# Kernel optimization log

Measured on AMD Instinct MI355X. Metric: run time of the kernel, lower is better.

The kernel has to match this reference:

```python
import jax, jax.numpy as jnp
import numpy as np
import math

D_MODEL = 1024
N_HEADS = 16
D_HEAD = D_MODEL // N_HEADS
D_FF = 4 * D_MODEL
EPS = 1e-5


def layer_norm(x, gamma, beta):
    mu = jnp.mean(x, axis=-1, keepdims=True)
    var = jnp.var(x, axis=-1, keepdims=True)
    return (x - mu) * jax.lax.rsqrt(var + EPS) * gamma + beta


def setup_inputs() -> dict:
    key = jax.random.key(0)
    ks = jax.random.split(key, 8)
    B, C, D = 32, 256, D_MODEL
    s = 0.02
    return {
        "X": jax.random.normal(ks[0], (B, C, D), dtype=jnp.float32),
        "W_qkv": jax.random.normal(ks[1], (D, 3 * D), dtype=jnp.float32) * s,
        "b_qkv": jnp.zeros((3 * D,), dtype=jnp.float32),
        "W_proj": jax.random.normal(ks[2], (D, D), dtype=jnp.float32) * s,
        "b_proj": jnp.zeros((D,), dtype=jnp.float32),
        "g1": jnp.ones((D,), dtype=jnp.float32),
        "beta1": jnp.zeros((D,), dtype=jnp.float32),
        "g2": jnp.ones((D,), dtype=jnp.float32),
        "beta2": jnp.zeros((D,), dtype=jnp.float32),
        "W_ff1": jax.random.normal(ks[3], (D, D_FF), dtype=jnp.float32) * s,
        "b_ff1": jnp.zeros((D_FF,), dtype=jnp.float32),
        "W_ff2": jax.random.normal(ks[4], (D_FF, D), dtype=jnp.float32) * s,
        "b_ff2": jnp.zeros((D,), dtype=jnp.float32),
    }


def reference(X, W_qkv, b_qkv, W_proj, b_proj, g1, beta1, g2, beta2,
              W_ff1, b_ff1, W_ff2, b_ff2):
    B, C, D = X.shape
    H, Dh = N_HEADS, D_HEAD
    scale = 1.0 / math.sqrt(Dh)

    Xn = layer_norm(X, g1, beta1)
    qkv = Xn @ W_qkv + b_qkv                       # [B, C, 3D]
    q, k, v = jnp.split(qkv, 3, axis=-1)
    # split heads -> [B, H, C, Dh]
    sh = lambda t: t.reshape(B, C, H, Dh).transpose(0, 2, 1, 3)
    q, k, v = sh(q), sh(k), sh(v)

    scores = jnp.einsum("bhcd,bhkd->bhck", q, k) * scale  # [B, H, C, C]
    attn = jax.nn.softmax(scores, axis=-1)
    ctx = jnp.einsum("bhck,bhkd->bhcd", attn, v)           # [B, H, C, Dh]
    ctx = ctx.transpose(0, 2, 1, 3).reshape(B, C, D)

    X1 = X + (ctx @ W_proj + b_proj)
    X2n = layer_norm(X1, g2, beta2)
    h = jax.nn.gelu(X2n @ W_ff1 + b_ff1, approximate=False)
    X_out = X1 + (h @ W_ff2 + b_ff2)
    A = attn.mean(axis=1)                                   # [B, C, C]
    return (X_out, A)
```

## Files before the change

### kernel.cpp

```cpp
#include <hip/hip_runtime.h>
#include <cstdint>
#include <cstddef>

typedef short bf16x8 __attribute__((ext_vector_type(8)));
typedef float f32x4 __attribute__((ext_vector_type(4)));
typedef unsigned short u16;
typedef u16 u16x8 __attribute__((ext_vector_type(8)));

#define GLD16(gptr, lptr)                                                            \
  __builtin_amdgcn_global_load_lds((const __attribute__((address_space(1))) void*)(gptr), \
                                   (__attribute__((address_space(3))) void*)(lptr), 16, 0, 0)

__device__ __forceinline__ u16 f2bf(float f) {
  union { float f; unsigned u; } v; v.f = f;
  unsigned r = v.u + 0x7FFF + ((v.u >> 16) & 1);
  return (u16)(r >> 16);
}
__device__ __forceinline__ float bf2f(u16 h) {
  union { unsigned u; float f; } v; v.u = ((unsigned)h) << 16;
  return v.f;
}

template <int N> __device__ __forceinline__ void vmwait() {
  if constexpr (N == 0) asm volatile("s_waitcnt vmcnt(0)" ::: "memory");
  else if constexpr (N == 2) asm volatile("s_waitcnt vmcnt(2)" ::: "memory");
  else asm volatile("s_waitcnt vmcnt(8)" ::: "memory");
}

__device__ __forceinline__ f32x4 mfma16(bf16x8 a, bf16x8 b, f32x4 c) {
  return __builtin_amdgcn_mfma_f32_16x16x32_bf16(a, b, c, 0, 0, 0);
}

__device__ __forceinline__ bf16x8 lds_read_sw64(const u16* base, int row, int col) {
  int byt = row * 128 + col * 2;
  byt ^= (row & 7) << 4;
  return *(const bf16x8*)((const char*)base + byt);
}

__global__ __launch_bounds__(256) void transpose_cast(const float* __restrict__ in,
                                                      u16* __restrict__ out, int R, int C) {
  __shared__ float tile[32][33];
  const int tx = threadIdx.x, ty = threadIdx.y;
  const int c0 = blockIdx.x * 32, r0 = blockIdx.y * 32;
#pragma unroll
  for (int i = 0; i < 32; i += 8)
    tile[ty + i][tx] = in[(size_t)(r0 + ty + i) * C + c0 + tx];
  __syncthreads();
#pragma unroll
  for (int i = 0; i < 32; i += 8)
    out[(size_t)(c0 + ty + i) * R + r0 + tx] = f2bf(tile[tx][ty + i]);
}

__global__ __launch_bounds__(256) void layernorm_bf16(const float* __restrict__ X,
                                                      const float* __restrict__ g,
                                                      const float* __restrict__ be,
                                                      u16* __restrict__ out) {
  const int row = blockIdx.x, t = threadIdx.x;
  const int lane = t & 63, wave = t >> 6;
  const float* x = X + (size_t)row * 1024;
  __shared__ float part[4];
  float v[4]; float s = 0.f;
#pragma unroll
  for (int i = 0; i < 4; ++i) { v[i] = x[t + i * 256]; s += v[i]; }
#pragma unroll
  for (int o = 32; o >= 1; o >>= 1) s += __shfl_xor(s, o);
  if (lane == 0) part[wave] = s;
  __syncthreads();
  const float mu = (part[0] + part[1] + part[2] + part[3]) * (1.f / 1024.f);
  float d2 = 0.f;
#pragma unroll
  for (int i = 0; i < 4; ++i) { float d = v[i] - mu; d2 += d * d; }
#pragma unroll
  for (int o = 32; o >= 1; o >>= 1) d2 += __shfl_xor(d2, o);
  __syncthreads();
  if (lane == 0) part[wave] = d2;
  __syncthreads();
  const float var = (part[0] + part[1] + part[2] + part[3]) * (1.f / 1024.f);
  const float rstd = rsqrtf(var + 1e-5f);
#pragma unroll
  for (int i = 0; i < 4; ++i) {
    const int c = t + i * 256;
    out[(size_t)row * 1024 + c] = f2bf((v[i] - mu) * rstd * g[c] + be[c]);
  }
}

template <int EPI>
__global__ __launch_bounds__(512, 2) void gemm_4p(const u16* __restrict__ A,
                                                  const u16* __restrict__ Bt,
                                                  const float* __restrict__ bias,
                                                  const float* __restrict__ res,
                                                  float* __restrict__ outf,
                                                  u16* __restrict__ outb,
                                                  int M, int N, int K) {
  constexpr int TSZ = 256 * 128;
  __shared__ __attribute__((aligned(16))) char lds[4 * TSZ];

  const int t = threadIdx.x, lane = t & 63, wave = t >> 6;
  const int wm = wave >> 2, wn = wave & 3;
  const int l15 = lane & 15, l16 = lane >> 4;

  const int lb = ((int)blockIdx.x & 7) * ((int)gridDim.x >> 3) + ((int)blockIdx.x >> 3);
  const int NBN = N >> 8;
  const int bm = (lb / NBN) * 256, bn = (lb % NBN) * 256;

  const u16* aptr[4];
  const u16* bptr[4];
#pragma unroll
  for (int u = 0; u < 4; ++u) {
    int Lb = u * 8192 + t * 16;
    int x = (Lb ^ ((Lb >> 3) & 0x70)) >> 1;
    aptr[u] = A + (size_t)(bm + (x >> 6)) * K + (x & 63);
    bptr[u] = Bt + (size_t)(bn + (x >> 6)) * K + (x & 63);
  }
  auto stA = [&](int p, int u) { GLD16(aptr[u] + p * 64, lds + (p & 1) * TSZ + u * 8192 + t * 16); };
  auto stB = [&](int p, int u) { GLD16(bptr[u] + p * 64, lds + 2 * TSZ + (p & 1) * TSZ + u * 8192 + t * 16); };

  stA(0, 0); stA(0, 2); stB(0, 0); stB(0, 1); stB(0, 2); stB(0, 3); stA(0, 1); stA(0, 3);

  f32x4 acc[8][4] = {};
  const int nkt = K >> 6;

#pragma unroll 1
  for (int kt = 0; kt < nkt; ++kt) {
    const char* ab = lds + (kt & 1) * TSZ;
    const char* bb = lds + 2 * TSZ + (kt & 1) * TSZ;
    const bool st = (kt + 1 < nkt);
    bf16x8 aF[4][2], b0[2][2], b1[2][2];

    vmwait<2>();
    asm volatile("s_barrier" ::: "memory");
    if (st) { stA(kt + 1, 0); stA(kt + 1, 2); stB(kt + 1, 0); stB(kt + 1, 1); }
#pragma unroll
    for (int fm = 0; fm < 4; ++fm) {
      const int r = wm * 128 + fm * 16 + l15;
      const int rb = r * 128, sw = (r & 7) << 4;
      aF[fm][0] = *(const bf16x8*)(ab + rb + ((l16 * 16) ^ sw));
      aF[fm][1] = *(const bf16x8*)(ab + rb + ((64 + l16 * 16) ^ sw));
    }
#pragma unroll
    for (int fn = 0; fn < 2; ++fn) {
      const int r = wn * 64 + fn * 16 + l15;
      const int rb = r * 128, sw = (r & 7) << 4;
      b0[fn][0] = *(const bf16x8*)(bb + rb + ((l16 * 16) ^ sw));
      b0[fn][1] = *(const bf16x8*)(bb + rb + ((64 + l16 * 16) ^ sw));
    }
    asm volatile("s_waitcnt lgkmcnt(0)" ::: "memory");
    __builtin_amdgcn_sched_barrier(0);
    __builtin_amdgcn_s_setprio(1);
#pragma unroll
    for (int ks = 0; ks < 2; ++ks)
#pragma unroll
      for (int fm = 0; fm < 4; ++fm)
#pragma unroll
        for (int fn = 0; fn < 2; ++fn)
          acc[fm][fn] = mfma16(aF[fm][ks], b0[fn][ks], acc[fm][fn]);
    __builtin_amdgcn_s_setprio(0);

    asm volatile("s_barrier" ::: "memory");
    if (st) { stB(kt + 1, 2); stB(kt + 1, 3); stA(kt + 1, 1); stA(kt + 1, 3); }
#pragma unroll
    for (int fn = 0; fn < 2; ++fn) {
      const int r = wn * 64 + (2 + fn) * 16 + l15;
      const int rb = r * 128, sw = (r & 7) << 4;
      b1[fn][0] = *(const bf16x8*)(bb + rb + ((l16 * 16) ^ sw));
      b1[fn][1] = *(const bf16x8*)(bb + rb + ((64 + l16 * 16) ^ sw));
    }
    asm volatile("s_waitcnt lgkmcnt(0)" ::: "memory");
    __builtin_amdgcn_sched_barrier(0);
    __builtin_amdgcn_s_setprio(1);
#pragma unroll
    for (int ks = 0; ks < 2; ++ks)
#pragma unroll
      for (int fm = 0; fm < 4; ++fm)
#pragma unroll
        for (int fn = 0; fn < 2; ++fn)
          acc[fm][2 + fn] = mfma16(aF[fm][ks], b1[fn][ks], acc[fm][2 + fn]);
    __builtin_amdgcn_s_setprio(0);

    if (st) vmwait<8>(); else vmwait<0>();
    asm volatile("s_barrier" ::: "memory");
#pragma unroll
    for (int fm = 0; fm < 4; ++fm) {
      const int r = wm * 128 + (4 + fm) * 16 + l15;
      const int rb = r * 128, sw = (r & 7) << 4;
      aF[fm][0] = *(const bf16x8*)(ab + rb + ((l16 * 16) ^ sw));
      aF[fm][1] = *(const bf16x8*)(ab + rb + ((64 + l16 * 16) ^ sw));
    }
    asm volatile("s_waitcnt lgkmcnt(0)" ::: "memory");
    __builtin_amdgcn_sched_barrier(0);
    __builtin_amdgcn_s_setprio(1);
#pragma unroll
    for (int ks = 0; ks < 2; ++ks)
#pragma unroll
      for (int fm = 0; fm < 4; ++fm)
#pragma unroll
        for (int fn = 0; fn < 2; ++fn)
          acc[4 + fm][2 + fn] = mfma16(aF[fm][ks], b1[fn][ks], acc[4 + fm][2 + fn]);
    __builtin_amdgcn_s_setprio(0);

    __builtin_amdgcn_s_setprio(1);
#pragma unroll
    for (int ks = 0; ks < 2; ++ks)
#pragma unroll
      for (int fm = 0; fm < 4; ++fm)
#pragma unroll
        for (int fn = 0; fn < 2; ++fn)
          acc[4 + fm][fn] = mfma16(aF[fm][ks], b0[fn][ks], acc[4 + fm][fn]);
    __builtin_amdgcn_s_setprio(0);
  }

  const int r0 = l16 * 4;
#pragma unroll
  for (int fm = 0; fm < 8; ++fm) {
#pragma unroll
    for (int fn = 0; fn < 4; ++fn) {
      const int col = bn + wn * 64 + fn * 16 + l15;
      const float bv = bias[col];
#pragma unroll
      for (int r = 0; r < 4; ++r) {
        const int row = bm + wm * 128 + fm * 16 + r0 + r;
        const float v = acc[fm][fn][r] + bv;
        const size_t o = (size_t)row * N + col;
        if (EPI == 0) {
          outb[o] = f2bf(v);
        } else if (EPI == 1) {
          outf[o] = res[o] + v;
        } else {
          const float u = 0.7978845608f * (v + 0.044715f * v * v * v);
          const float e = __expf(2.f * u);
          const float th = 1.f - 2.f / (1.f + e);
          outb[o] = f2bf(0.5f * v * (1.f + th));
        }
      }
    }
  }
}

template <int EPI>
__global__ __launch_bounds__(256, 2) void gemm_sb(const u16* __restrict__ A,
                                                  const u16* __restrict__ Bt,
                                                  const float* __restrict__ bias,
                                                  const float* __restrict__ res,
                                                  float* __restrict__ outf,
                                                  u16* __restrict__ outb,
                                                  int M, int N, int K) {
  constexpr int ABYT = 128 * 128;
  __shared__ __attribute__((aligned(16))) char lds[2 * ABYT];

  const int t = threadIdx.x, lane = t & 63, wave = t >> 6;
  const int wm = wave >> 1, wn = wave & 1;
  const int l15 = lane & 15, l16 = lane >> 4;

  const int xcd = (int)blockIdx.x & 7, q = (int)blockIdx.x >> 3;
  const int j = q & 63, gq = q >> 6;
  const int g = gq * 8 + xcd;
  const int NGN = N >> 10;
  const int gm = g / NGN, gn = g % NGN;
  const int bm = (gm * 8 + (j >> 3)) * 128;
  const int bn = (gn * 8 + (j & 7)) * 128;

  const u16* aptr[4];
  const u16* bptr[4];
#pragma unroll
  for (int c = 0; c < 4; ++c) {
    int Lb = c * 4096 + t * 16;
    int x = (Lb ^ ((Lb >> 3) & 0x70)) >> 1;
    aptr[c] = A + (size_t)(bm + (x >> 6)) * K + (x & 63);
    bptr[c] = Bt + (size_t)(bn + (x >> 6)) * K + (x & 63);
  }

  auto stage = [&](int p) {
    const int ko = p * 64;
    char* ab = lds + t * 16;
    char* bb = lds + ABYT + t * 16;
#pragma unroll
    for (int c = 0; c < 4; ++c) GLD16(aptr[c] + ko, ab + c * 4096);
#pragma unroll
    for (int c = 0; c < 4; ++c) GLD16(bptr[c] + ko, bb + c * 4096);
  };

  const int co0 = l16 * 16, co1 = 64 + l16 * 16;
  f32x4 acc[4][4] = {};
  const int nkt = K >> 6;

#pragma unroll 1
  for (int kt = 0; kt < nkt; ++kt) {
    __syncthreads();
    stage(kt);
    __syncthreads();

    const char* ab = lds;
    const char* bb = lds + ABYT;
#pragma unroll
    for (int ks = 0; ks < 2; ++ks) {
      const int co = ks ? co1 : co0;
      bf16x8 a[4], b[4];
#pragma unroll
      for (int m = 0; m < 4; ++m) {
        const int r = wm * 64 + m * 16 + l15;
        a[m] = *(const bf16x8*)(ab + r * 128 + (co ^ ((r & 7) << 4)));
      }
#pragma unroll
      for (int n = 0; n < 4; ++n) {
        const int r = wn * 64 + n * 16 + l15;
        b[n] = *(const bf16x8*)(bb + r * 128 + (co ^ ((r & 7) << 4)));
      }
#pragma unroll
      for (int m = 0; m < 4; ++m)
#pragma unroll
        for (int n = 0; n < 4; ++n)
          acc[m][n] = mfma16(a[m], b[n], acc[m][n]);
    }
  }

  const int r0 = l16 * 4;
#pragma unroll
  for (int m = 0; m < 4; ++m) {
#pragma unroll
    for (int n = 0; n < 4; ++n) {
      const int col = bn + wn * 64 + n * 16 + l15;
      const float bv = bias[col];
#pragma unroll
      for (int r = 0; r < 4; ++r) {
        const int row = bm + wm * 64 + m * 16 + r0 + r;
        const float v = acc[m][n][r] + bv;
        const size_t o = (size_t)row * N + col;
        if (EPI == 0) {
          outb[o] = f2bf(v);
        } else if (EPI == 1) {
          outf[o] = res[o] + v;
        } else {
          const float u = 0.7978845608f * (v + 0.044715f * v * v * v);
          const float e = __expf(2.f * u);
          const float th = 1.f - 2.f / (1.f + e);
          outb[o] = f2bf(0.5f * v * (1.f + th));
        }
      }
    }
  }
}

__global__ __launch_bounds__(256) void attn_scores(const u16* __restrict__ qkv,
                                                   u16* __restrict__ probs) {
  __shared__ u16 Ks[256 * 64];
  __shared__ u16 Qs[64 * 64];
  const int t = threadIdx.x, lane = t & 63, wave = t >> 6;
  const int qb = blockIdx.x * 64, h = blockIdx.y, b = blockIdx.z;
  const size_t row0 = (size_t)b * 256 * 3072;

#pragma unroll
  for (int is = 0; is < 8; ++is) {
    int L = (is * 2048 + t * 8) * 2;
    int x = (L ^ ((L >> 3) & 0x70)) >> 1;
    int kk = x >> 6, d = x & 63;
    const u16* gp = qkv + row0 + (size_t)kk * 3072 + 1024 + h * 64 + d;
    GLD16(gp, (char*)Ks + is * 4096 + wave * 1024);
  }
#pragma unroll
  for (int is = 0; is < 2; ++is) {
    int L = (is * 2048 + t * 8) * 2;
    int x = (L ^ ((L >> 3) & 0x70)) >> 1;
    int q = x >> 6, d = x & 63;
    const u16* gp = qkv + row0 + (size_t)(qb + q) * 3072 + h * 64 + d;
    GLD16(gp, (char*)Qs + is * 4096 + wave * 1024);
  }
  __syncthreads();

  f32x4 acc[16] = {};
  bf16x8 aq[2];
#pragma unroll
  for (int ks = 0; ks < 2; ++ks)
    aq[ks] = lds_read_sw64(Qs, wave * 16 + (lane & 15), ks * 32 + (lane >> 4) * 8);
#pragma unroll
  for (int nf = 0; nf < 16; ++nf) {
#pragma unroll
    for (int ks = 0; ks < 2; ++ks) {
      bf16x8 bk = lds_read_sw64(Ks, nf * 16 + (lane & 15), ks * 32 + (lane >> 4) * 8);
      acc[nf] = mfma16(aq[ks], bk, acc[nf]);
    }
  }

  const int r0 = (lane >> 4) * 4, cc = lane & 15;
  const float sc = 0.125f;
#pragma unroll
  for (int r = 0; r < 4; ++r) {
    float mx = -1e30f;
#pragma unroll
    for (int nf = 0; nf < 16; ++nf) mx = fmaxf(mx, acc[nf][r]);
#pragma unroll
    for (int o = 8; o >= 1; o >>= 1) mx = fmaxf(mx, __shfl_xor(mx, o));
    float s = 0.f;
#pragma unroll
    for (int nf = 0; nf < 16; ++nf) {
      float e = __expf((acc[nf][r] - mx) * sc);
      acc[nf][r] = e; s += e;
    }
#pragma unroll
    for (int o = 8; o >= 1; o >>= 1) s += __shfl_xor(s, o);
    const float rinv = 1.f / s;
    const int qrow = qb + wave * 16 + r0 + r;
    u16* prow = probs + (size_t)((b * 16 + h) * 256 + qrow) * 256;
#pragma unroll
    for (int nf = 0; nf < 16; ++nf)
      prow[nf * 16 + cc] = f2bf(acc[nf][r] * rinv);
  }
}

__global__ __launch_bounds__(256) void amean(const u16* __restrict__ probs,
                                             float* __restrict__ A) {
  const int bq = blockIdx.x;
  const int b = bq >> 8, q = bq & 255;
  const int t = threadIdx.x;
  float s = 0.f;
#pragma unroll
  for (int h = 0; h < 16; ++h)
    s += bf2f(probs[(size_t)((b * 16 + h) * 256 + q) * 256 + t]);
  A[(size_t)bq * 256 + t] = s * (1.f / 16.f);
}

__global__ __launch_bounds__(256) void attn_pv(const u16* __restrict__ qkv,
                                               const u16* __restrict__ probs,
                                               u16* __restrict__ ctx) {
  __shared__ u16 Vs[64 * 256];
  const int t = threadIdx.x, lane = t & 63, wave = t >> 6;
  const int h = blockIdx.x, b = blockIdx.y;

#pragma unroll
  for (int p = 0; p < 8; ++p) {
    int idx = p * 2048 + t * 8;
    int kk = idx >> 6, d0 = idx & 63;
    u16x8 vv = *(const u16x8*)(qkv + (size_t)(b * 256 + kk) * 3072 + 2048 + h * 64 + d0);
#pragma unroll
    for (int j = 0; j < 8; ++j) {
      int d = d0 + j;
      int byt = (d * 512 + kk * 2) ^ ((d & 7) << 4);
      *(u16*)((char*)Vs + byt) = vv[j];
    }
  }
  __syncthreads();

  f32x4 acc[4][4] = {};
  const u16* Pb = probs + (size_t)((b * 16 + h) * 256) * 256;
  const int cc = lane & 15, kg = (lane >> 4) * 8;
#pragma unroll
  for (int kt = 0; kt < 8; ++kt) {
    bf16x8 a[4], v[4];
#pragma unroll
    for (int m = 0; m < 4; ++m)
      a[m] = *(const bf16x8*)(Pb + (size_t)(wave * 64 + m * 16 + cc) * 256 + kt * 32 + kg);
#pragma unroll
    for (int n = 0; n < 4; ++n) {
      int d = n * 16 + cc;
      int kk = kt * 32 + kg;
      int byt = (d * 512 + kk * 2) ^ ((d & 7) << 4);
      v[n] = *(const bf16x8*)((const char*)Vs + byt);
    }
#pragma unroll
    for (int m = 0; m < 4; ++m)
#pragma unroll
      for (int n = 0; n < 4; ++n)
        acc[m][n] = mfma16(a[m], v[n], acc[m][n]);
  }

  const int r0 = (lane >> 4) * 4;
#pragma unroll
  for (int m = 0; m < 4; ++m) {
    const int q = wave * 64 + m * 16 + r0;
#pragma unroll
    for (int n = 0; n < 4; ++n) {
      const int col = h * 64 + n * 16 + cc;
#pragma unroll
      for (int r = 0; r < 4; ++r)
        ctx[(size_t)(b * 256 + q + r) * 1024 + col] = f2bf(acc[m][n][r]);
    }
  }
}

extern "C" void kernel_launch(void* const* d_in, const int* in_sizes, int n_in,
                              void* d_out, int out_size, void* d_ws, size_t ws_size,
                              hipStream_t stream) {
  const float* X      = (const float*)d_in[0];
  const float* W_qkv  = (const float*)d_in[1];
  const float* b_qkv  = (const float*)d_in[2];
  const float* W_proj = (const float*)d_in[3];
  const float* b_proj = (const float*)d_in[4];
  const float* g1     = (const float*)d_in[5];
  const float* beta1  = (const float*)d_in[6];
  const float* g2     = (const float*)d_in[7];
  const float* beta2  = (const float*)d_in[8];
  const float* W_ff1  = (const float*)d_in[9];
  const float* b_ff1  = (const float*)d_in[10];
  const float* W_ff2  = (const float*)d_in[11];
  const float* b_ff2  = (const float*)d_in[12];

  float* Xout = (float*)d_out;
  float* Aout = (float*)d_out + 8388608;

  char* ws = (char*)d_ws;
  const size_t MB = 1u << 20;
  u16* xn    = (u16*)(ws + 0);
  u16* wqkv  = (u16*)(ws + 16 * MB);
  u16* wproj = (u16*)(ws + 22 * MB);
  u16* wff1  = (u16*)(ws + 24 * MB);
  u16* wff2  = (u16*)(ws + 32 * MB);
  u16* qkv   = (u16*)(ws + 40 * MB);
  u16* probs = (u16*)(ws + 88 * MB);
  u16* hbuf  = probs;
  float* x1  = (float*)(ws + 152 * MB);
  u16* ctx   = xn;
  u16* x1n   = xn;

  const dim3 tb(32, 8);
  transpose_cast<<<dim3(96, 32),  tb, 0, stream>>>(W_qkv,  wqkv, 1024, 3072);
  transpose_cast<<<dim3(32, 32),  tb, 0, stream>>>(W_proj, wproj, 1024, 1024);
  transpose_cast<<<dim3(128, 32), tb, 0, stream>>>(W_ff1,  wff1, 1024, 4096);
  transpose_cast<<<dim3(32, 128), tb, 0, stream>>>(W_ff2,  wff2, 4096, 1024);

  layernorm_bf16<<<8192, 256, 0, stream>>>(X, g1, beta1, xn);

  gemm_4p<0><<<384, 512, 0, stream>>>(xn, wqkv, b_qkv, nullptr, nullptr, qkv,
                                      8192, 3072, 1024);

  attn_scores<<<dim3(4, 16, 32), 256, 0, stream>>>(qkv, probs);
  amean<<<8192, 256, 0, stream>>>(probs, Aout);
  attn_pv<<<dim3(16, 32), 256, 0, stream>>>(qkv, probs, ctx);

  gemm_sb<1><<<512, 256, 0, stream>>>(ctx, wproj, b_proj, X, x1, nullptr,
                                      8192, 1024, 1024);

  layernorm_bf16<<<8192, 256, 0, stream>>>(x1, g2, beta2, x1n);

  gemm_4p<2><<<512, 512, 0, stream>>>(x1n, wff1, b_ff1, nullptr, nullptr, hbuf,
                                      8192, 4096, 1024);

  gemm_sb<1><<<512, 256, 0, stream>>>(hbuf, wff2, b_ff2, x1, Xout, nullptr,
                                      8192, 1024, 4096);
}
```

Measured before the change: 357.4 us.

## Restructure 256x256 GEMM main loop into 8-phase schedule over two K tiles

Replaces the 4-phase per-K-tile GEMM loop with an 8-phase loop that processes two K tiles per iteration. Each phase reads a pair of A fragments, issues one half-tile of global-to-LDS prefetch, and runs 16 MFMAs. B tiles are prefetched one tile further ahead than A. The aim is to spread loads and barriers more evenly and deepen prefetch to hide memory latency, at the cost of more barriers per tile and tighter wait-count reasoning. The loop assumes K is a multiple of 128, which holds for K=1024.

```diff
diff --git a/kernel.cpp b/kernel.cpp
--- a/kernel.cpp
+++ b/kernel.cpp
@@ -23,7 +23,7 @@
 
 template <int N> __device__ __forceinline__ void vmwait() {
   if constexpr (N == 0) asm volatile("s_waitcnt vmcnt(0)" ::: "memory");
-  else if constexpr (N == 2) asm volatile("s_waitcnt vmcnt(2)" ::: "memory");
+  else if constexpr (N == 4) asm volatile("s_waitcnt vmcnt(4)" ::: "memory");
   else asm volatile("s_waitcnt vmcnt(8)" ::: "memory");
 }
 
@@ -85,15 +85,17 @@
 }
 
 template <int EPI>
-__global__ __launch_bounds__(512, 2) void gemm_4p(const u16* __restrict__ A,
-                                                  const u16* __restrict__ Bt,
-                                                  const float* __restrict__ bias,
-                                                  const float* __restrict__ res,
-                                                  float* __restrict__ outf,
-                                                  u16* __restrict__ outb,
-                                                  int M, int N, int K) {
+__global__ __launch_bounds__(512, 2) void gemm_8ph(const u16* __restrict__ A,
+                                                   const u16* __restrict__ Bt,
+                                                   const float* __restrict__ bias,
+                                                   const float* __restrict__ res,
+                                                   float* __restrict__ outf,
+                                                   u16* __restrict__ outb,
+                                                   int M, int N, int K) {
   constexpr int TSZ = 256 * 128;
   __shared__ __attribute__((aligned(16))) char lds[4 * TSZ];
+  char* ldsA = lds;
+  char* ldsB = lds + 2 * TSZ;
 
   const int t = threadIdx.x, lane = t & 63, wave = t >> 6;
   const int wm = wave >> 2, wn = wave & 3;
@@ -112,101 +114,113 @@
     aptr[u] = A + (size_t)(bm + (x >> 6)) * K + (x & 63);
     bptr[u] = Bt + (size_t)(bn + (x >> 6)) * K + (x & 63);
   }
-  auto stA = [&](int p, int u) { GLD16(aptr[u] + p * 64, lds + (p & 1) * TSZ + u * 8192 + t * 16); };
-  auto stB = [&](int p, int u) { GLD16(bptr[u] + p * 64, lds + 2 * TSZ + (p & 1) * TSZ + u * 8192 + t * 16); };
-
-  stA(0, 0); stA(0, 2); stB(0, 0); stB(0, 1); stB(0, 2); stB(0, 3); stA(0, 1); stA(0, 3);
+  auto stA_ = [&](int tile, int half) {
+    char* d = ldsA + (tile & 1) * TSZ + half * 16384 + t * 16;
+    GLD16(aptr[half * 2 + 0] + tile * 64, d);
+    GLD16(aptr[half * 2 + 1] + tile * 64, d + 8192);
+  };
+  auto stB_ = [&](int tile, int half) {
+    char* d = ldsB + (tile & 1) * TSZ + half * 16384 + t * 16;
+    GLD16(bptr[half * 2 + 0] + tile * 64, d);
+    GLD16(bptr[half * 2 + 1] + tile * 64, d + 8192);
+  };
+
+  auto rdA = [&](const char* ab, int fm, bf16x8 (&o)[2]) {
+    const int r = wm * 128 + fm * 16 + l15;
+    const int rb = r * 128, sw = (r & 7) << 4;
+    o[0] = *(const bf16x8*)(ab + rb + ((l16 * 16) ^ sw));
+    o[1] = *(const bf16x8*)(ab + rb + ((64 + l16 * 16) ^ sw));
+  };
+  auto rdB = [&](const char* bb, int fn, bf16x8 (&o)[2]) {
+    const int r = wn * 64 + fn * 16 + l15;
+    const int rb = r * 128, sw = (r & 7) << 4;
+    o[0] = *(const bf16x8*)(bb + rb + ((l16 * 16) ^ sw));
+    o[1] = *(const bf16x8*)(bb + rb + ((64 + l16 * 16) ^ sw));
+  };
+
+  const int nkt = K >> 6;
+  const int nit = nkt >> 1;
+
+  stB_(0, 0); stB_(0, 1); stA_(0, 0); stA_(0, 1);
+  stB_(1, 0); stB_(1, 1);
+  vmwait<4>();
+  asm volatile("s_barrier" ::: "memory");
 
   f32x4 acc[8][4] = {};
-  const int nkt = K >> 6;
 
 #pragma unroll 1
-  for (int kt = 0; kt < nkt; ++kt) {
-    const char* ab = lds + (kt & 1) * TSZ;
-    const char* bb = lds + 2 * TSZ + (kt & 1) * TSZ;
-    const bool st = (kt + 1 < nkt);
-    bf16x8 aF[4][2], b0[2][2], b1[2][2];
-
-    vmwait<2>();
-    asm volatile("s_barrier" ::: "memory");
-    if (st) { stA(kt + 1, 0); stA(kt + 1, 2); stB(kt + 1, 0); stB(kt + 1, 1); }
-#pragma unroll
-    for (int fm = 0; fm < 4; ++fm) {
-      const int r = wm * 128 + fm * 16 + l15;
-      const int rb = r * 128, sw = (r & 7) << 4;
-      aF[fm][0] = *(const bf16x8*)(ab + rb + ((l16 * 16) ^ sw));
-      aF[fm][1] = *(const bf16x8*)(ab + rb + ((64 + l16 * 16) ^ sw));
-    }
-#pragma unroll
-    for (int fn = 0; fn < 2; ++fn) {
-      const int r = wn * 64 + fn * 16 + l15;
-      const int rb = r * 128, sw = (r & 7) << 4;
-      b0[fn][0] = *(const bf16x8*)(bb + rb + ((l16 * 16) ^ sw));
-      b0[fn][1] = *(const bf16x8*)(bb + rb + ((64 + l16 * 16) ^ sw));
-    }
-    asm volatile("s_waitcnt lgkmcnt(0)" ::: "memory");
-    __builtin_amdgcn_sched_barrier(0);
-    __builtin_amdgcn_s_setprio(1);
-#pragma unroll
-    for (int ks = 0; ks < 2; ++ks)
-#pragma unroll
-      for (int fm = 0; fm < 4; ++fm)
-#pragma unroll
-        for (int fn = 0; fn < 2; ++fn)
-          acc[fm][fn] = mfma16(aF[fm][ks], b0[fn][ks], acc[fm][fn]);
-    __builtin_amdgcn_s_setprio(0);
-
-    asm volatile("s_barrier" ::: "memory");
-    if (st) { stB(kt + 1, 2); stB(kt + 1, 3); stA(kt + 1, 1); stA(kt + 1, 3); }
-#pragma unroll
-    for (int fn = 0; fn < 2; ++fn) {
-      const int r = wn * 64 + (2 + fn) * 16 + l15;
-      const int rb = r * 128, sw = (r & 7) << 4;
-      b1[fn][0] = *(const bf16x8*)(bb + rb + ((l16 * 16) ^ sw));
-      b1[fn][1] = *(const bf16x8*)(bb + rb + ((64 + l16 * 16) ^ sw));
-    }
-    asm volatile("s_waitcnt lgkmcnt(0)" ::: "memory");
-    __builtin_amdgcn_sched_barrier(0);
-    __builtin_amdgcn_s_setprio(1);
-#pragma unroll
-    for (int ks = 0; ks < 2; ++ks)
-#pragma unroll
-      for (int fm = 0; fm < 4; ++fm)
-#pragma unroll
-        for (int fn = 0; fn < 2; ++fn)
-          acc[fm][2 + fn] = mfma16(aF[fm][ks], b1[fn][ks], acc[fm][2 + fn]);
-    __builtin_amdgcn_s_setprio(0);
-
-    if (st) vmwait<8>(); else vmwait<0>();
-    asm volatile("s_barrier" ::: "memory");
-#pragma unroll
-    for (int fm = 0; fm < 4; ++fm) {
-      const int r = wm * 128 + (4 + fm) * 16 + l15;
-      const int rb = r * 128, sw = (r & 7) << 4;
-      aF[fm][0] = *(const bf16x8*)(ab + rb + ((l16 * 16) ^ sw));
-      aF[fm][1] = *(const bf16x8*)(ab + rb + ((64 + l16 * 16) ^ sw));
-    }
-    asm volatile("s_waitcnt lgkmcnt(0)" ::: "memory");
-    __builtin_amdgcn_sched_barrier(0);
-    __builtin_amdgcn_s_setprio(1);
-#pragma unroll
-    for (int ks = 0; ks < 2; ++ks)
-#pragma unroll
-      for (int fm = 0; fm < 4; ++fm)
-#pragma unroll
-        for (int fn = 0; fn < 2; ++fn)
-          acc[4 + fm][2 + fn] = mfma16(aF[fm][ks], b1[fn][ks], acc[4 + fm][2 + fn]);
-    __builtin_amdgcn_s_setprio(0);
-
-    __builtin_amdgcn_s_setprio(1);
-#pragma unroll
-    for (int ks = 0; ks < 2; ++ks)
-#pragma unroll
-      for (int fm = 0; fm < 4; ++fm)
-#pragma unroll
-        for (int fn = 0; fn < 2; ++fn)
-          acc[4 + fm][fn] = mfma16(aF[fm][ks], b0[fn][ks], acc[4 + fm][fn]);
-    __builtin_amdgcn_s_setprio(0);
+  for (int it = 0; it < nit; ++it) {
+    const int T0 = 2 * it;
+    const bool s2 = (T0 + 2 < nkt);
+    const bool s3 = (T0 + 3 < nkt);
+
+    {
+      const char* ab = ldsA + (T0 & 1) * TSZ;
+      const char* bb = ldsB + (T0 & 1) * TSZ;
+      bf16x8 Bh[4][2];
+#pragma unroll
+      for (int fmp = 0; fmp < 4; ++fmp) {
+        bf16x8 A0[2], A1[2];
+        rdA(ab, fmp * 2 + 0, A0);
+        rdA(ab, fmp * 2 + 1, A1);
+        if (fmp == 0) {
+#pragma unroll
+          for (int fn = 0; fn < 4; ++fn) rdB(bb, fn, Bh[fn]);
+        }
+        if (fmp == 0) stA_(T0 + 1, 0);
+        else if (fmp == 1) stA_(T0 + 1, 1);
+        else if (fmp == 2) { if (s2) stB_(T0 + 2, 0); }
+        else               { if (s2) stB_(T0 + 2, 1); }
+        asm volatile("s_barrier" ::: "memory");
+        asm volatile("s_waitcnt lgkmcnt(0)" ::: "memory");
+        __builtin_amdgcn_sched_barrier(0);
+        __builtin_amdgcn_s_setprio(1);
+#pragma unroll
+        for (int ks = 0; ks < 2; ++ks)
+#pragma unroll
+          for (int fn = 0; fn < 4; ++fn) {
+            acc[fmp * 2 + 0][fn] = mfma16(A0[ks], Bh[fn][ks], acc[fmp * 2 + 0][fn]);
+            acc[fmp * 2 + 1][fn] = mfma16(A1[ks], Bh[fn][ks], acc[fmp * 2 + 1][fn]);
+          }
+        __builtin_amdgcn_s_setprio(0);
+        if (fmp == 3) { if (s2) vmwait<4>(); else vmwait<0>(); }
+        asm volatile("s_barrier" ::: "memory");
+      }
+    }
+
+    {
+      const char* ab = ldsA + ((T0 + 1) & 1) * TSZ;
+      const char* bb = ldsB + ((T0 + 1) & 1) * TSZ;
+      bf16x8 Bh[4][2];
+#pragma unroll
+      for (int fmp = 0; fmp < 4; ++fmp) {
+        bf16x8 A0[2], A1[2];
+        rdA(ab, fmp * 2 + 0, A0);
+        rdA(ab, fmp * 2 + 1, A1);
+        if (fmp == 0) {
+#pragma unroll
+          for (int fn = 0; fn < 4; ++fn) rdB(bb, fn, Bh[fn]);
+        }
+        if (fmp == 0)      { if (s2) stA_(T0 + 2, 0); }
+        else if (fmp == 1) { if (s2) stA_(T0 + 2, 1); }
+        else if (fmp == 2) { if (s3) stB_(T0 + 3, 0); }
+        else               { if (s3) stB_(T0 + 3, 1); }
+        asm volatile("s_barrier" ::: "memory");
+        asm volatile("s_waitcnt lgkmcnt(0)" ::: "memory");
+        __builtin_amdgcn_sched_barrier(0);
+        __builtin_amdgcn_s_setprio(1);
+#pragma unroll
+        for (int ks = 0; ks < 2; ++ks)
+#pragma unroll
+          for (int fn = 0; fn < 4; ++fn) {
+            acc[fmp * 2 + 0][fn] = mfma16(A0[ks], Bh[fn][ks], acc[fmp * 2 + 0][fn]);
+            acc[fmp * 2 + 1][fn] = mfma16(A1[ks], Bh[fn][ks], acc[fmp * 2 + 1][fn]);
+          }
+        __builtin_amdgcn_s_setprio(0);
+        if (fmp == 3) { if (s2) vmwait<4>(); else vmwait<0>(); }
+        asm volatile("s_barrier" ::: "memory");
+      }
+    }
   }
 
   const int r0 = l16 * 4;
@@ -518,8 +532,8 @@
 
   layernorm_bf16<<<8192, 256, 0, stream>>>(X, g1, beta1, xn);
 
-  gemm_4p<0><<<384, 512, 0, stream>>>(xn, wqkv, b_qkv, nullptr, nullptr, qkv,
-                                      8192, 3072, 1024);
+  gemm_8ph<0><<<384, 512, 0, stream>>>(xn, wqkv, b_qkv, nullptr, nullptr, qkv,
+                                       8192, 3072, 1024);
 
   attn_scores<<<dim3(4, 16, 32), 256, 0, stream>>>(qkv, probs);
   amean<<<8192, 256, 0, stream>>>(probs, Aout);
@@ -530,8 +544,8 @@
 
   layernorm_bf16<<<8192, 256, 0, stream>>>(x1, g2, beta2, x1n);
 
-  gemm_4p<2><<<512, 512, 0, stream>>>(x1n, wff1, b_ff1, nullptr, nullptr, hbuf,
-                                      8192, 4096, 1024);
+  gemm_8ph<2><<<512, 512, 0, stream>>>(x1n, wff1, b_ff1, nullptr, nullptr, hbuf,
+                                       8192, 4096, 1024);
 
   gemm_sb<1><<<512, 256, 0, stream>>>(hbuf, wff2, b_ff2, x1, Xout, nullptr,
                                       8192, 1024, 4096);
```

New measurement: 357.8 us. About the same (+0.1%).
